# Kernel optimization log

Hardware: AMD Instinct MI355X
Metric: run time of the kernel (lower is better)

## Reference

```python
import jax, jax.numpy as jnp
import numpy as np

N_NODES = 50000
N_EDGES = 800000
N_GRAPHS = 8
D_IN, D_HID, D_OUT = 128, 128, 64


def setup_inputs() -> dict:
    key = jax.random.key(0)
    ks = jax.random.split(key, 8)
    x = jax.random.normal(ks[0], (N_NODES, D_IN), jnp.float32)
    src = jax.random.randint(ks[1], (N_EDGES,), 0, N_NODES, dtype=jnp.int32)
    dst = jax.random.randint(ks[2], (N_EDGES,), 0, N_NODES, dtype=jnp.int32)
    graph_id = jnp.sort(jax.random.randint(ks[3], (N_NODES,), 0, N_GRAPHS, dtype=jnp.int32))
    s1 = 1.0 / np.sqrt(D_IN)
    s2 = 1.0 / np.sqrt(D_HID)
    W1 = jax.random.normal(ks[4], (D_IN, D_HID), jnp.float32) * s1
    b1 = jnp.zeros((D_HID,), jnp.float32)
    W2 = jax.random.normal(ks[5], (D_HID, D_HID), jnp.float32) * s2
    b2 = jnp.zeros((D_HID,), jnp.float32)
    Wl = jax.random.normal(ks[6], (D_HID, D_OUT), jnp.float32) * s2
    bl = jnp.zeros((D_OUT,), jnp.float32)
    return dict(x=x, W1=W1, b1=b1, W2=W2, b2=b2, Wl=Wl, bl=bl,
                src=src, dst=dst, graph_id=graph_id)


def _graph_conv(x, W, b, src, dst):
    # DGL GraphConv, norm='both': h' = D_in^{-1/2} A (D_out^{-1/2} x W) + b
    n = x.shape[0]
    ones = jnp.ones((src.shape[0],), x.dtype)
    out_deg = jax.ops.segment_sum(ones, src, num_segments=n)
    in_deg = jax.ops.segment_sum(ones, dst, num_segments=n)
    norm_src = jax.lax.rsqrt(jnp.clip(out_deg, 1.0))  # [N]
    norm_dst = jax.lax.rsqrt(jnp.clip(in_deg, 1.0))   # [N]
    h = (x * norm_src[:, None]) @ W                    # [N, D]
    agg = jax.ops.segment_sum(h[src], dst, num_segments=n)  # gather-scatter SpMM
    return agg * norm_dst[:, None] + b


def reference(x, W1, b1, W2, b2, Wl, bl, src, dst, graph_id):
    h = jax.nn.relu(_graph_conv(x, W1, b1, src, dst))
    h = _graph_conv(h, W2, b2, src, dst)
    # dgl.mean_nodes over batched graph: per-graph mean of node features
    cnt = jax.ops.segment_sum(jnp.ones((x.shape[0],), x.dtype), graph_id,
                              num_segments=N_GRAPHS)
    pooled = jax.ops.segment_sum(h, graph_id, num_segments=N_GRAPHS)
    means = pooled / jnp.clip(cnt, 1.0)[:, None]       # [B, D_HID]
    return means @ Wl + bl                              # [B, D_OUT]
```

## Files before the change

kernel.cpp:

```cpp
#include <hip/hip_runtime.h>
#include <hip/hip_bf16.h>

#define N_NODES 50000
#define N_EDGES 800000
#define N_GRAPHS 8
#define MAXDEG 64
#define NRANGE 4
#define NCHUNK 64
#define RSZ (N_NODES / NRANGE)
#define CHE (N_EDGES / NCHUNK)

typedef __attribute__((ext_vector_type(8))) short short8;
typedef __attribute__((ext_vector_type(4))) float floatx4;
typedef __attribute__((ext_vector_type(2))) float floatx2;

static __device__ __forceinline__ ushort f2b(float f) {
    union { float f; unsigned u; } v; v.f = f;
    return (ushort)((v.u + 0x7FFF + ((v.u >> 16) & 1)) >> 16);
}
static __device__ __forceinline__ float b2f(unsigned u) {
    union { unsigned u; float f; } v; v.u = u << 16;
    return v.f;
}
static __device__ __forceinline__ unsigned char f2q(float f) {
    int p = __builtin_amdgcn_cvt_pk_fp8_f32(f, f, 0, false);
    return (unsigned char)(p & 0xff);
}

__global__ __launch_bounds__(1024) void prep_kernel(
    const int* __restrict__ src, const int* __restrict__ dst,
    const float* __restrict__ W1, const float* __restrict__ W2,
    const int* __restrict__ gid,
    ushort* __restrict__ counts_in, ushort* __restrict__ counts_out,
    ushort* __restrict__ Wt1, ushort* __restrict__ Wt2,
    int* __restrict__ start)
{
    int b = blockIdx.x, t = threadIdx.x;
    if (b < 256) {
        __shared__ unsigned h[RSZ];
        int c = b & (NCHUNK - 1), r = b >> 6;
        int lo = r * RSZ;
        for (int j = t; j < RSZ; j += 1024) h[j] = 0;
        __syncthreads();
        int ebeg = c * CHE, eend = ebeg + CHE;
        for (int i = ebeg + t; i < eend; i += 1024) {
            int s = src[i], d = dst[i];
            unsigned ds = (unsigned)(d - lo);
            if (ds < RSZ) atomicAdd(&h[ds >> 1], 1u << ((ds & 1) * 16));
            unsigned ss = (unsigned)(s - lo);
            if (ss < RSZ) atomicAdd(&h[(RSZ / 2) + (ss >> 1)], 1u << ((ss & 1) * 16));
        }
        __syncthreads();
        unsigned* ci = (unsigned*)(counts_in  + (size_t)c * N_NODES + lo);
        unsigned* co = (unsigned*)(counts_out + (size_t)c * N_NODES + lo);
        for (int j = t; j < RSZ / 2; j += 1024) {
            ci[j] = h[j];
            co[j] = h[(RSZ / 2) + j];
        }
    } else if (b < 272) {
        int i = (b - 256) * 1024 + t;
        int c = i >> 7, k = i & 127;
        Wt1[i] = f2b(W1[k * 128 + c]);
        Wt2[i] = f2b(W2[k * 128 + c]);
    } else {
        int i = (b - 272) * 1024 + t;
        if (i < N_NODES) {
            int g = gid[i];
            int gp = (i == 0) ? -1 : gid[i - 1];
            for (int k = gp + 1; k <= g; ++k) start[k] = i;
            if (i == N_NODES - 1)
                for (int k = g + 1; k <= N_GRAPHS; ++k) start[k] = N_NODES;
        }
    }
}

__global__ __launch_bounds__(256) void scan_kernel(
    const ushort* __restrict__ counts_in, const ushort* __restrict__ counts_out,
    ushort* __restrict__ base, int* __restrict__ in_deg,
    float* __restrict__ ns, float* __restrict__ nd)
{
    int v = blockIdx.x * 256 + threadIdx.x;
    if (v >= N_NODES) return;
    unsigned od = 0;
    #pragma unroll 8
    for (int c = 0; c < NCHUNK; ++c) od += counts_out[(size_t)c * N_NODES + v];
    unsigned run = 0;
    #pragma unroll 8
    for (int c = 0; c < NCHUNK; ++c) {
        base[(size_t)c * N_NODES + v] = (ushort)run;
        run += counts_in[(size_t)c * N_NODES + v];
    }
    in_deg[v] = (int)run;
    ns[v] = rsqrtf(fmaxf((float)od, 1.f));
    nd[v] = rsqrtf(fmaxf((float)run, 1.f));
}

__global__ __launch_bounds__(1024) void scatter_kernel(
    const int* __restrict__ src, const int* __restrict__ dst,
    const ushort* __restrict__ base, ushort* __restrict__ slot)
{
    __shared__ unsigned h[RSZ / 2];
    int t = threadIdx.x;
    int c = blockIdx.x & (NCHUNK - 1), r = blockIdx.x >> 6;
    int lo = r * RSZ;
    const unsigned* bp = (const unsigned*)(base + (size_t)c * N_NODES + lo);
    for (int j = t; j < RSZ / 2; j += 1024) h[j] = bp[j];
    __syncthreads();
    int ebeg = c * CHE, eend = ebeg + CHE;
    for (int i = ebeg + t; i < eend; i += 1024) {
        int d = dst[i];
        unsigned ds = (unsigned)(d - lo);
        if (ds < RSZ) {
            int sh = (ds & 1) * 16;
            unsigned old = atomicAdd(&h[ds >> 1], 1u << sh);
            unsigned pos = (old >> sh) & 0xffff;
            if (pos < MAXDEG) slot[(size_t)d * MAXDEG + pos] = (ushort)src[i];
        }
    }
}

template<int FP32_IN>
__global__ __launch_bounds__(256, 2) void mfma_gemm_kernel(
    const void* __restrict__ Xv, const float* __restrict__ scale,
    const ushort* __restrict__ Wt, unsigned char* __restrict__ Y, int n)
{
    int t = threadIdx.x;
    int wv = t >> 6, lane = t & 63;
    int m = lane & 15, q = lane >> 4;
    short8 B[8][4];
    #pragma unroll
    for (int cb = 0; cb < 8; ++cb)
        #pragma unroll
        for (int kb = 0; kb < 4; ++kb)
            B[cb][kb] = *(const short8*)&Wt[(size_t)(cb * 16 + m) * 128 + kb * 32 + q * 8];

    int ntile = n >> 4;
    int gw = blockIdx.x * 4 + wv;
    for (int tile = gw; tile < ntile; tile += 2048) {
        int row = tile * 16 + m;
        short8 a[4];
        if (FP32_IN) {
            const float* X = (const float*)Xv;
            float s = scale[row];
            #pragma unroll
            for (int kb = 0; kb < 4; ++kb) {
                const float* p = X + (size_t)row * 128 + kb * 32 + q * 8;
                float4 f0 = *(const float4*)p;
                float4 f1 = *(const float4*)(p + 4);
                short8 av;
                av[0] = (short)f2b(f0.x * s); av[1] = (short)f2b(f0.y * s);
                av[2] = (short)f2b(f0.z * s); av[3] = (short)f2b(f0.w * s);
                av[4] = (short)f2b(f1.x * s); av[5] = (short)f2b(f1.y * s);
                av[6] = (short)f2b(f1.z * s); av[7] = (short)f2b(f1.w * s);
                a[kb] = av;
            }
        } else {
            const ushort* X = (const ushort*)Xv;
            #pragma unroll
            for (int kb = 0; kb < 4; ++kb)
                a[kb] = *(const short8*)(X + (size_t)row * 128 + kb * 32 + q * 8);
        }
        floatx4 acc[8] = {};
        #pragma unroll
        for (int cb = 0; cb < 8; ++cb)
            #pragma unroll
            for (int kb = 0; kb < 4; ++kb)
                acc[cb] = __builtin_amdgcn_mfma_f32_16x16x32_bf16(a[kb], B[cb][kb], acc[cb], 0, 0, 0);
        int rowbase = tile * 16 + q * 4;
        #pragma unroll
        for (int cb = 0; cb < 8; ++cb)
            #pragma unroll
            for (int r = 0; r < 4; ++r)
                Y[(size_t)(rowbase + r) * 128 + cb * 16 + m] = f2q(acc[cb][r]);
    }
}

__global__ __launch_bounds__(256) void spmm_fp8_kernel(
    const unsigned char* __restrict__ H, const int* __restrict__ in_deg,
    const ushort* __restrict__ slot, const float* __restrict__ norm_dst,
    const float* __restrict__ norm_src, const float* __restrict__ bias,
    ushort* __restrict__ Y, int n, int relu_scale)
{
    int w = (blockIdx.x * blockDim.x + threadIdx.x) >> 6;
    int lane = threadIdx.x & 63;
    if (w >= n) return;
    int cnt = min(in_deg[w], MAXDEG);
    const ushort* lst = slot + (size_t)w * MAXDEG;
    int g = lane >> 4;
    int c8 = (lane & 15) * 8;
    int myslot = lst[lane];
    float acc[8] = {};
    for (int e = 0; e < cnt; e += 4) {
        int idx = e + g;
        bool ok = idx < cnt;
        int s = __shfl(myslot, ok ? idx : 0, 64);
        if (ok) {
            uint2 v = *(const uint2*)&H[(size_t)s * 128 + c8];
            floatx2 p01 = __builtin_amdgcn_cvt_pk_f32_fp8((int)v.x, false);
            floatx2 p23 = __builtin_amdgcn_cvt_pk_f32_fp8((int)v.x, true);
            floatx2 p45 = __builtin_amdgcn_cvt_pk_f32_fp8((int)v.y, false);
            floatx2 p67 = __builtin_amdgcn_cvt_pk_f32_fp8((int)v.y, true);
            acc[0] += p01.x; acc[1] += p01.y;
            acc[2] += p23.x; acc[3] += p23.y;
            acc[4] += p45.x; acc[5] += p45.y;
            acc[6] += p67.x; acc[7] += p67.y;
        }
    }
    #pragma unroll
    for (int j = 0; j < 8; ++j) {
        acc[j] += __shfl_xor(acc[j], 16, 64);
        acc[j] += __shfl_xor(acc[j], 32, 64);
    }
    float ndv = norm_dst[w];
    float4 b0 = *(const float4*)&bias[c8];
    float4 b1 = *(const float4*)&bias[c8 + 4];
    float r[8];
    r[0] = acc[0] * ndv + b0.x; r[1] = acc[1] * ndv + b0.y;
    r[2] = acc[2] * ndv + b0.z; r[3] = acc[3] * ndv + b0.w;
    r[4] = acc[4] * ndv + b1.x; r[5] = acc[5] * ndv + b1.y;
    r[6] = acc[6] * ndv + b1.z; r[7] = acc[7] * ndv + b1.w;
    if (relu_scale) {
        float nsv = norm_src[w];
        #pragma unroll
        for (int j = 0; j < 8; ++j) r[j] = fmaxf(r[j], 0.f) * nsv;
    }
    if (lane < 16) {
        uint4 o;
        o.x = (unsigned)f2b(r[0]) | ((unsigned)f2b(r[1]) << 16);
        o.y = (unsigned)f2b(r[2]) | ((unsigned)f2b(r[3]) << 16);
        o.z = (unsigned)f2b(r[4]) | ((unsigned)f2b(r[5]) << 16);
        o.w = (unsigned)f2b(r[6]) | ((unsigned)f2b(r[7]) << 16);
        *(uint4*)&Y[(size_t)w * 128 + c8] = o;
    }
}

__global__ __launch_bounds__(256) void pool_kernel(
    const ushort* __restrict__ H, const int* __restrict__ start,
    float* __restrict__ part)
{
    __shared__ float red[128];
    int t = threadIdx.x;
    int g = blockIdx.x >> 5, j = blockIdx.x & 31;
    int beg0 = start[g], len = start[g + 1] - beg0;
    int sbeg = beg0 + (int)(((long long)len * j) >> 5);
    int send = beg0 + (int)(((long long)len * (j + 1)) >> 5);
    int wv = t >> 6, lane = t & 63;
    int rg = lane >> 4;
    int c8 = (lane & 15) * 8;
    float acc[8] = {};
    for (int v = sbeg + wv * 4 + rg; v < send; v += 16) {
        uint4 u = *(const uint4*)&H[(size_t)v * 128 + c8];
        acc[0] += b2f(u.x & 0xffff); acc[1] += b2f(u.x >> 16);
        acc[2] += b2f(u.y & 0xffff); acc[3] += b2f(u.y >> 16);
        acc[4] += b2f(u.z & 0xffff); acc[5] += b2f(u.z >> 16);
        acc[6] += b2f(u.w & 0xffff); acc[7] += b2f(u.w >> 16);
    }
    #pragma unroll
    for (int k = 0; k < 8; ++k) {
        acc[k] += __shfl_xor(acc[k], 16, 64);
        acc[k] += __shfl_xor(acc[k], 32, 64);
    }
    if (t < 128) red[t] = 0.f;
    __syncthreads();
    if (lane < 16) {
        #pragma unroll
        for (int k = 0; k < 8; ++k) atomicAdd(&red[c8 + k], acc[k]);
    }
    __syncthreads();
    if (t < 128) part[(size_t)blockIdx.x * 128 + t] = red[t];
}

__global__ __launch_bounds__(512) void head_kernel(
    const float* __restrict__ part, const int* __restrict__ start,
    const float* __restrict__ Wl, const float* __restrict__ bl,
    float* __restrict__ out)
{
    __shared__ float means[N_GRAPHS * 128];
    int t = threadIdx.x;
    for (int i = t; i < N_GRAPHS * 128; i += 512) {
        int g = i >> 7, k = i & 127;
        float s = 0.f;
        #pragma unroll 8
        for (int j = 0; j < 32; ++j) s += part[(size_t)(g * 32 + j) * 128 + k];
        float cnt = (float)(start[g + 1] - start[g]);
        means[i] = s / fmaxf(cnt, 1.f);
    }
    __syncthreads();
    int g = t >> 6, c = t & 63;
    float acc = bl[c];
    #pragma unroll 8
    for (int k = 0; k < 128; ++k)
        acc = fmaf(means[g * 128 + k], Wl[k * 64 + c], acc);
    out[g * 64 + c] = acc;
}

extern "C" void kernel_launch(void* const* d_in, const int* in_sizes, int n_in,
                              void* d_out, int out_size, void* d_ws, size_t ws_size,
                              hipStream_t stream) {
    const float* x   = (const float*)d_in[0];
    const float* W1  = (const float*)d_in[1];
    const float* b1  = (const float*)d_in[2];
    const float* W2  = (const float*)d_in[3];
    const float* b2  = (const float*)d_in[4];
    const float* Wl  = (const float*)d_in[5];
    const float* bl  = (const float*)d_in[6];
    const int*   src = (const int*)d_in[7];
    const int*   dst = (const int*)d_in[8];
    const int*   gid = (const int*)d_in[9];

    const int n = N_NODES;

    char* ws = (char*)d_ws;
    size_t off = 0;
    auto alloc = [&](size_t bytes) { size_t o = off; off += (bytes + 255) & ~(size_t)255; return o; };
    unsigned char* hA = (unsigned char*)(ws + alloc((size_t)n * 128));
    ushort* hB        = (ushort*)(ws + alloc((size_t)n * 128 * 2));
    ushort* slot      = (ushort*)(ws + alloc((size_t)n * MAXDEG * 2));
    ushort* counts_in = (ushort*)(ws + alloc((size_t)NCHUNK * n * 2));
    ushort* counts_out= (ushort*)(ws + alloc((size_t)NCHUNK * n * 2));
    ushort* basev     = (ushort*)(ws + alloc((size_t)NCHUNK * n * 2));
    float* norm_src   = (float*) (ws + alloc((size_t)n * 4));
    float* norm_dst   = (float*) (ws + alloc((size_t)n * 4));
    int*   in_deg     = (int*)   (ws + alloc((size_t)n * 4));
    int*   startb     = (int*)   (ws + alloc((size_t)(N_GRAPHS + 1) * 4));
    ushort* Wt1       = (ushort*)(ws + alloc((size_t)128 * 128 * 2));
    ushort* Wt2       = (ushort*)(ws + alloc((size_t)128 * 128 * 2));
    float* part       = (float*) (ws + alloc((size_t)N_GRAPHS * 32 * 128 * 4));

    int spmm_blocks = (n + 3) / 4;

    prep_kernel<<<321, 1024, 0, stream>>>(src, dst, W1, W2, gid,
                                          counts_in, counts_out, Wt1, Wt2, startb);
    scan_kernel<<<(n + 255) / 256, 256, 0, stream>>>(counts_in, counts_out, basev,
                                                     in_deg, norm_src, norm_dst);
    scatter_kernel<<<NRANGE * NCHUNK, 1024, 0, stream>>>(src, dst, basev, slot);
    mfma_gemm_kernel<1><<<512, 256, 0, stream>>>(x, norm_src, Wt1, hA, n);
    spmm_fp8_kernel<<<spmm_blocks, 256, 0, stream>>>(hA, in_deg, slot, norm_dst,
                                                     norm_src, b1, hB, n, 1);
    mfma_gemm_kernel<0><<<512, 256, 0, stream>>>(hB, nullptr, Wt2, hA, n);
    spmm_fp8_kernel<<<spmm_blocks, 256, 0, stream>>>(hA, in_deg, slot, norm_dst,
                                                     nullptr, b2, hB, n, 0);
    pool_kernel<<<N_GRAPHS * 32, 256, 0, stream>>>(hB, startb, part);
    head_kernel<<<1, 512, 0, stream>>>(part, startb, Wl, bl, (float*)d_out);
}
```

Baseline: 213.4 us.

## Process eight destination nodes per wavefront in fp8 SpMM with 16-byte gathers

Restructures the SpMM so each 64-lane wavefront handles eight destination nodes, with eight lanes per node each loading 16 fp8 features (uint4) per neighbor. Before, one wavefront served one node with four edge groups and needed a cross-lane reduction. The new layout removes that reduction, widens the loads and writes every lane's output. In exchange, lanes in a wavefront sit idle while the node with the most neighbors (up to 64) finishes, and the launch grid now depends on N_NODES being divisible by 8.

After: 199.7 us. -6.4%, faster.

```diff
diff --git a/kernel.cpp b/kernel.cpp
--- a/kernel.cpp
+++ b/kernel.cpp
@@ -179,59 +179,71 @@
     const unsigned char* __restrict__ H, const int* __restrict__ in_deg,
     const ushort* __restrict__ slot, const float* __restrict__ norm_dst,
     const float* __restrict__ norm_src, const float* __restrict__ bias,
-    ushort* __restrict__ Y, int n, int relu_scale)
-{
-    int w = (blockIdx.x * blockDim.x + threadIdx.x) >> 6;
+    ushort* __restrict__ Y, int relu_scale)
+{
+    int wid = (blockIdx.x * blockDim.x + threadIdx.x) >> 6;
+    if (wid >= N_NODES / 8) return;
     int lane = threadIdx.x & 63;
-    if (w >= n) return;
-    int cnt = min(in_deg[w], MAXDEG);
-    const ushort* lst = slot + (size_t)w * MAXDEG;
-    int g = lane >> 4;
-    int c8 = (lane & 15) * 8;
-    int myslot = lst[lane];
-    float acc[8] = {};
-    for (int e = 0; e < cnt; e += 4) {
-        int idx = e + g;
-        bool ok = idx < cnt;
-        int s = __shfl(myslot, ok ? idx : 0, 64);
-        if (ok) {
-            uint2 v = *(const uint2*)&H[(size_t)s * 128 + c8];
-            floatx2 p01 = __builtin_amdgcn_cvt_pk_f32_fp8((int)v.x, false);
-            floatx2 p23 = __builtin_amdgcn_cvt_pk_f32_fp8((int)v.x, true);
-            floatx2 p45 = __builtin_amdgcn_cvt_pk_f32_fp8((int)v.y, false);
-            floatx2 p67 = __builtin_amdgcn_cvt_pk_f32_fp8((int)v.y, true);
-            acc[0] += p01.x; acc[1] += p01.y;
-            acc[2] += p23.x; acc[3] += p23.y;
-            acc[4] += p45.x; acc[5] += p45.y;
-            acc[6] += p67.x; acc[7] += p67.y;
-        }
-    }
+    int g = lane >> 3;
+    int j = lane & 7;
+    int node = wid * 8 + g;
+    int cnt = min(in_deg[node], MAXDEG);
+    float ndv = norm_dst[node];
+    const ushort* lst = slot + (size_t)node * MAXDEG;
+
+    int cm = cnt;
+    cm = max(cm, __shfl_xor(cm, 8, 64));
+    cm = max(cm, __shfl_xor(cm, 16, 64));
+    cm = max(cm, __shfl_xor(cm, 32, 64));
+
+    float acc[16] = {};
+    for (int e0 = 0; e0 < cm; e0 += 8) {
+        int sl = lst[e0 + j];
+        #pragma unroll
+        for (int k = 0; k < 8; ++k) {
+            if (e0 + k < cnt) {
+                int s = __shfl(sl, g * 8 + k, 64);
+                uint4 v = *(const uint4*)&H[(size_t)s * 128 + j * 16];
+                floatx2 p;
+                p = __builtin_amdgcn_cvt_pk_f32_fp8((int)v.x, false); acc[0] += p.x;  acc[1] += p.y;
+                p = __builtin_amdgcn_cvt_pk_f32_fp8((int)v.x, true);  acc[2] += p.x;  acc[3] += p.y;
+                p = __builtin_amdgcn_cvt_pk_f32_fp8((int)v.y, false); acc[4] += p.x;  acc[5] += p.y;
+                p = __builtin_amdgcn_cvt_pk_f32_fp8((int)v.y, true);  acc[6] += p.x;  acc[7] += p.y;
+                p = __builtin_amdgcn_cvt_pk_f32_fp8((int)v.z, false); acc[8] += p.x;  acc[9] += p.y;
+                p = __builtin_amdgcn_cvt_pk_f32_fp8((int)v.z, true);  acc[10] += p.x; acc[11] += p.y;
+                p = __builtin_amdgcn_cvt_pk_f32_fp8((int)v.w, false); acc[12] += p.x; acc[13] += p.y;
+                p = __builtin_amdgcn_cvt_pk_f32_fp8((int)v.w, true);  acc[14] += p.x; acc[15] += p.y;
+            }
+        }
+    }
+
+    int c16 = j * 16;
+    float r[16];
     #pragma unroll
-    for (int j = 0; j < 8; ++j) {
-        acc[j] += __shfl_xor(acc[j], 16, 64);
-        acc[j] += __shfl_xor(acc[j], 32, 64);
-    }
-    float ndv = norm_dst[w];
-    float4 b0 = *(const float4*)&bias[c8];
-    float4 b1 = *(const float4*)&bias[c8 + 4];
-    float r[8];
-    r[0] = acc[0] * ndv + b0.x; r[1] = acc[1] * ndv + b0.y;
-    r[2] = acc[2] * ndv + b0.z; r[3] = acc[3] * ndv + b0.w;
-    r[4] = acc[4] * ndv + b1.x; r[5] = acc[5] * ndv + b1.y;
-    r[6] = acc[6] * ndv + b1.z; r[7] = acc[7] * ndv + b1.w;
+    for (int u = 0; u < 4; ++u) {
+        float4 bv = *(const float4*)&bias[c16 + u * 4];
+        r[u * 4 + 0] = acc[u * 4 + 0] * ndv + bv.x;
+        r[u * 4 + 1] = acc[u * 4 + 1] * ndv + bv.y;
+        r[u * 4 + 2] = acc[u * 4 + 2] * ndv + bv.z;
+        r[u * 4 + 3] = acc[u * 4 + 3] * ndv + bv.w;
+    }
     if (relu_scale) {
-        float nsv = norm_src[w];
-        #pragma unroll
-        for (int j = 0; j < 8; ++j) r[j] = fmaxf(r[j], 0.f) * nsv;
-    }
-    if (lane < 16) {
-        uint4 o;
-        o.x = (unsigned)f2b(r[0]) | ((unsigned)f2b(r[1]) << 16);
-        o.y = (unsigned)f2b(r[2]) | ((unsigned)f2b(r[3]) << 16);
-        o.z = (unsigned)f2b(r[4]) | ((unsigned)f2b(r[5]) << 16);
-        o.w = (unsigned)f2b(r[6]) | ((unsigned)f2b(r[7]) << 16);
-        *(uint4*)&Y[(size_t)w * 128 + c8] = o;
-    }
+        float nsv = norm_src[node];
+        #pragma unroll
+        for (int u = 0; u < 16; ++u) r[u] = fmaxf(r[u], 0.f) * nsv;
+    }
+    uint4 o0, o1;
+    o0.x = (unsigned)f2b(r[0])  | ((unsigned)f2b(r[1])  << 16);
+    o0.y = (unsigned)f2b(r[2])  | ((unsigned)f2b(r[3])  << 16);
+    o0.z = (unsigned)f2b(r[4])  | ((unsigned)f2b(r[5])  << 16);
+    o0.w = (unsigned)f2b(r[6])  | ((unsigned)f2b(r[7])  << 16);
+    o1.x = (unsigned)f2b(r[8])  | ((unsigned)f2b(r[9])  << 16);
+    o1.y = (unsigned)f2b(r[10]) | ((unsigned)f2b(r[11]) << 16);
+    o1.z = (unsigned)f2b(r[12]) | ((unsigned)f2b(r[13]) << 16);
+    o1.w = (unsigned)f2b(r[14]) | ((unsigned)f2b(r[15]) << 16);
+    uint4* yp = (uint4*)&Y[(size_t)node * 128 + c16];
+    yp[0] = o0;
+    yp[1] = o1;
 }
 
 __global__ __launch_bounds__(256) void pool_kernel(
@@ -327,7 +339,7 @@
     ushort* Wt2       = (ushort*)(ws + alloc((size_t)128 * 128 * 2));
     float* part       = (float*) (ws + alloc((size_t)N_GRAPHS * 32 * 128 * 4));
 
-    int spmm_blocks = (n + 3) / 4;
+    int spmm_blocks = (N_NODES / 8 + 3) / 4;
 
     prep_kernel<<<321, 1024, 0, stream>>>(src, dst, W1, W2, gid,
                                           counts_in, counts_out, Wt1, Wt2, startb);
@@ -336,10 +348,10 @@
     scatter_kernel<<<NRANGE * NCHUNK, 1024, 0, stream>>>(src, dst, basev, slot);
     mfma_gemm_kernel<1><<<512, 256, 0, stream>>>(x, norm_src, Wt1, hA, n);
     spmm_fp8_kernel<<<spmm_blocks, 256, 0, stream>>>(hA, in_deg, slot, norm_dst,
-                                                     norm_src, b1, hB, n, 1);
+                                                     norm_src, b1, hB, 1);
     mfma_gemm_kernel<0><<<512, 256, 0, stream>>>(hB, nullptr, Wt2, hA, n);
     spmm_fp8_kernel<<<spmm_blocks, 256, 0, stream>>>(hA, in_deg, slot, norm_dst,
-                                                     nullptr, b2, hB, n, 0);
+                                                     nullptr, b2, hB, 0);
     pool_kernel<<<N_GRAPHS * 32, 256, 0, stream>>>(hB, startb, part);
     head_kernel<<<1, 512, 0, stream>>>(part, startb, Wl, bl, (float*)d_out);
 }
```
